# Kernel tuning notes

Hardware: AMD Instinct MI355X
Metric: run time of the kernel (lower is better)

The kernel has to match this reference:

```python
import jax, jax.numpy as jnp
import numpy as np


def color_bin(x, n_bins):
    """Per-image 3D color histogram over n_bins**3 flat bins.
    x: [B, 3, H, W] float in ~[-1, 1]. Returns [B, n_bins**3] float32.
    """
    B, C, H, W = x.shape
    n_tot = n_bins ** 3
    # torch color_bins: i*(2/n_bins) - 1 for i in 1..n_bins-1
    boundaries = jnp.arange(1, n_bins, dtype=jnp.float32) * (2.0 / n_bins) - 1.0
    # torch.bucketize(right=False) == searchsorted side='left'
    idx = jnp.searchsorted(boundaries, x.reshape(B, C, H * W), side='left')  # [B,3,HW] int
    scale = jnp.array([1, n_bins, n_bins ** 2], dtype=idx.dtype)
    flat = jnp.einsum('bcp,c->bp', idx, scale)  # [B, HW], values in [0, n_tot)
    # torch.histc(bins, n_tot, min=0, max=n_tot-1) on exact integers == bincount
    hist = jax.vmap(lambda f: jnp.bincount(f, length=n_tot))(flat)
    return hist.astype(jnp.float32) / (H * W)


def setup_inputs() -> dict:
    key = jax.random.key(0)
    k1, k2 = jax.random.split(key)
    inp = jax.random.normal(k1, (8, 3, 1024, 1024), dtype=jnp.float32)
    style = jax.random.normal(k2, (1, 3, 1024, 1024), dtype=jnp.float32)
    return {"input": inp, "style_image": style, "n_bins": 16}


def reference(input, style_image, n_bins):
    # target histogram from the style image (detached in torch; ints anyway)
    target = color_bin(style_image, n_bins).squeeze(0)  # [n_tot]
    cols = color_bin(input, n_bins)                     # [B, n_tot]
    # F.l1_loss(cols, target.repeat(B, 1)) with mean reduction
    loss = jnp.mean(jnp.abs(cols - target[None, :]))
    return loss
```

## Files before the change

kernel.cpp:

```cpp
#include <hip/hip_runtime.h>

#define HW      (1024 * 1024)
#define HW4     (HW / 4)
#define NBINS   4096
#define NIMG    9
#define BPI     256
#define THREADS 256
#define F4_PER_BLOCK (HW4 / BPI)
#define NPART   (NIMG * BPI)

typedef float f4 __attribute__((ext_vector_type(4)));

__device__ __forceinline__ int bin16(float x) {
    int lo = 0;
    if (0.0f < x) lo = 8;
    if ((float)(lo + 4) * 0.125f - 1.0f < x) lo += 4;
    if ((float)(lo + 2) * 0.125f - 1.0f < x) lo += 2;
    if ((float)(lo + 1) * 0.125f - 1.0f < x) lo += 1;
    return lo;
}

__device__ __forceinline__ int bin3(float r, float g, float b) {
    return bin16(r) + 16 * bin16(g) + 256 * bin16(b);
}

__device__ __forceinline__ void acc4(int* lh, f4 r, f4 g, f4 b) {
    atomicAdd(&lh[bin3(r.x, g.x, b.x)], 1);
    atomicAdd(&lh[bin3(r.y, g.y, b.y)], 1);
    atomicAdd(&lh[bin3(r.z, g.z, b.z)], 1);
    atomicAdd(&lh[bin3(r.w, g.w, b.w)], 1);
}

__global__ __launch_bounds__(THREADS) void hist_kernel(
        const float* __restrict__ input,
        const float* __restrict__ style,
        unsigned int* __restrict__ part) {
    __shared__ int lh[NBINS];
    const int img = blockIdx.y;
    const int blk = blockIdx.x;
    const float* base = (img < 8) ? (input + (size_t)img * 3 * HW) : style;

    for (int i = threadIdx.x; i < NBINS; i += THREADS) lh[i] = 0;
    __syncthreads();

    const f4* c0 = (const f4*)(base);
    const f4* c1 = (const f4*)(base + HW);
    const f4* c2 = (const f4*)(base + 2 * HW);
    const int start = blk * F4_PER_BLOCK;

    for (int j = threadIdx.x; j < F4_PER_BLOCK; j += 2 * THREADS) {
        const int p0 = start + j;
        const int p1 = p0 + THREADS;
        f4 r0 = c0[p0], g0 = c1[p0], b0 = c2[p0];
        f4 r1 = c0[p1], g1 = c1[p1], b1 = c2[p1];
        acc4(lh, r0, g0, b0);
        acc4(lh, r1, g1, b1);
    }
    __syncthreads();

    uint2* dst = (uint2*)(part + ((size_t)img * BPI + blk) * (NBINS / 2));
    for (int i = threadIdx.x; i < NBINS / 4; i += THREADS) {
        uint2 v;
        v.x = (unsigned)lh[4 * i]     | ((unsigned)lh[4 * i + 1] << 16);
        v.y = (unsigned)lh[4 * i + 2] | ((unsigned)lh[4 * i + 3] << 16);
        dst[i] = v;
    }
}

__global__ __launch_bounds__(THREADS) void reduce_kernel(
        const unsigned short* __restrict__ part,
        int* __restrict__ H2) {
    const int img  = blockIdx.y;
    const int half = blockIdx.z;
    const int bin  = blockIdx.x * THREADS + threadIdx.x;
    const unsigned short* p = part
        + ((size_t)img * BPI + half * (BPI / 2)) * NBINS + bin;
    int sum = 0;
#pragma unroll 16
    for (int b = 0; b < BPI / 2; ++b) sum += p[(size_t)b * NBINS];
    H2[((size_t)half * NIMG + img) * NBINS + bin] = sum;
}

__global__ __launch_bounds__(1024) void loss_kernel(
        const int* __restrict__ H2, float* __restrict__ out) {
    __shared__ int tgt_l[NBINS];
    __shared__ int partsum[16];
    const int* h0 = H2;
    const int* h1 = H2 + NIMG * NBINS;
    for (int i = threadIdx.x; i < NBINS; i += 1024)
        tgt_l[i] = h0[8 * NBINS + i] + h1[8 * NBINS + i];
    __syncthreads();

    int acc = 0;
    for (int e = threadIdx.x; e < 8 * NBINS; e += 1024) {
        const int c = h0[e] + h1[e];
        const int d = c - tgt_l[e & (NBINS - 1)];
        acc += (d < 0) ? -d : d;
    }
    for (int off = 32; off; off >>= 1) acc += __shfl_down(acc, off, 64);
    const int lane = threadIdx.x & 63;
    const int wv   = threadIdx.x >> 6;
    if (lane == 0) partsum[wv] = acc;
    __syncthreads();
    if (wv == 0) {
        int t = (lane < 16) ? partsum[lane] : 0;
        for (int off = 8; off; off >>= 1) t += __shfl_down(t, off, 64);
        if (lane == 0) {
            out[0] = (float)((double)(long long)t / 34359738368.0);
        }
    }
}

extern "C" void kernel_launch(void* const* d_in, const int* in_sizes, int n_in,
                              void* d_out, int out_size, void* d_ws, size_t ws_size,
                              hipStream_t stream) {
    const float* input = (const float*)d_in[0];
    const float* style = (const float*)d_in[1];
    unsigned int* part = (unsigned int*)d_ws;
    int* H2 = (int*)((char*)d_ws + (size_t)NPART * NBINS * sizeof(unsigned short));

    hipLaunchKernelGGL(hist_kernel, dim3(BPI, NIMG), dim3(THREADS), 0, stream,
                       input, style, part);
    hipLaunchKernelGGL(reduce_kernel, dim3(NBINS / THREADS, NIMG, 2),
                       dim3(THREADS), 0, stream,
                       (const unsigned short*)part, H2);
    hipLaunchKernelGGL(loss_kernel, dim3(1), dim3(1024), 0, stream,
                       H2, (float*)d_out);
}
```

Baseline: 179.9 us.

## Halve hist blocks per image and fuse partial reduction with L1 loss

```diff
diff --git a/kernel.cpp b/kernel.cpp
--- a/kernel.cpp
+++ b/kernel.cpp
@@ -4,10 +4,10 @@
 #define HW4     (HW / 4)
 #define NBINS   4096
 #define NIMG    9
-#define BPI     256
+#define BPI     128
 #define THREADS 256
 #define F4_PER_BLOCK (HW4 / BPI)
-#define NPART   (NIMG * BPI)
+#define RBINS   32
 
 typedef float f4 __attribute__((ext_vector_type(4)));
 
@@ -34,7 +34,7 @@
 __global__ __launch_bounds__(THREADS) void hist_kernel(
         const float* __restrict__ input,
         const float* __restrict__ style,
-        unsigned int* __restrict__ part) {
+        unsigned short* __restrict__ part) {
     __shared__ int lh[NBINS];
     const int img = blockIdx.y;
     const int blk = blockIdx.x;
@@ -58,57 +58,61 @@
     }
     __syncthreads();
 
-    uint2* dst = (uint2*)(part + ((size_t)img * BPI + blk) * (NBINS / 2));
-    for (int i = threadIdx.x; i < NBINS / 4; i += THREADS) {
-        uint2 v;
-        v.x = (unsigned)lh[4 * i]     | ((unsigned)lh[4 * i + 1] << 16);
-        v.y = (unsigned)lh[4 * i + 2] | ((unsigned)lh[4 * i + 3] << 16);
+    uint4* dst = (uint4*)(part + ((size_t)img * BPI + blk) * NBINS);
+    for (int i = threadIdx.x; i < NBINS / 8; i += THREADS) {
+        uint4 v;
+        v.x = (unsigned)lh[8 * i]     | ((unsigned)lh[8 * i + 1] << 16);
+        v.y = (unsigned)lh[8 * i + 2] | ((unsigned)lh[8 * i + 3] << 16);
+        v.z = (unsigned)lh[8 * i + 4] | ((unsigned)lh[8 * i + 5] << 16);
+        v.w = (unsigned)lh[8 * i + 6] | ((unsigned)lh[8 * i + 7] << 16);
         dst[i] = v;
     }
 }
 
-__global__ __launch_bounds__(THREADS) void reduce_kernel(
+__global__ __launch_bounds__(THREADS) void reduce_loss_kernel(
         const unsigned short* __restrict__ part,
-        int* __restrict__ H2) {
-    const int img  = blockIdx.y;
-    const int half = blockIdx.z;
-    const int bin  = blockIdx.x * THREADS + threadIdx.x;
-    const unsigned short* p = part
-        + ((size_t)img * BPI + half * (BPI / 2)) * NBINS + bin;
-    int sum = 0;
+        int* __restrict__ slots) {
+    __shared__ int red[8][RBINS];
+    __shared__ int tgt[RBINS];
+    const int b0   = blockIdx.x * RBINS;
+    const int lane = threadIdx.x & 31;
+    const int pg   = threadIdx.x >> 5;
+    int acc = 0;
+
+    for (int step = 0; step < NIMG; ++step) {
+        const int img = (step == 0) ? 8 : step - 1;
+        const unsigned short* p =
+            part + ((size_t)img * BPI + pg) * NBINS + b0 + lane;
+        int s = 0;
 #pragma unroll 16
-    for (int b = 0; b < BPI / 2; ++b) sum += p[(size_t)b * NBINS];
-    H2[((size_t)half * NIMG + img) * NBINS + bin] = sum;
+        for (int k = 0; k < BPI / 8; ++k)
+            s += p[(size_t)(8 * k) * NBINS];
+        red[pg][lane] = s;
+        __syncthreads();
+        if (threadIdx.x < RBINS) {
+            int tot = 0;
+#pragma unroll
+            for (int r = 0; r < 8; ++r) tot += red[r][threadIdx.x];
+            if (step == 0) {
+                tgt[threadIdx.x] = tot;
+            } else {
+                const int d = tot - tgt[threadIdx.x];
+                acc += (d < 0) ? -d : d;
+            }
+        }
+        __syncthreads();
+    }
+
+    for (int off = 32; off; off >>= 1) acc += __shfl_down(acc, off, 64);
+    if (threadIdx.x == 0) slots[blockIdx.x] = acc;
 }
 
-__global__ __launch_bounds__(1024) void loss_kernel(
-        const int* __restrict__ H2, float* __restrict__ out) {
-    __shared__ int tgt_l[NBINS];
-    __shared__ int partsum[16];
-    const int* h0 = H2;
-    const int* h1 = H2 + NIMG * NBINS;
-    for (int i = threadIdx.x; i < NBINS; i += 1024)
-        tgt_l[i] = h0[8 * NBINS + i] + h1[8 * NBINS + i];
-    __syncthreads();
-
-    int acc = 0;
-    for (int e = threadIdx.x; e < 8 * NBINS; e += 1024) {
-        const int c = h0[e] + h1[e];
-        const int d = c - tgt_l[e & (NBINS - 1)];
-        acc += (d < 0) ? -d : d;
-    }
-    for (int off = 32; off; off >>= 1) acc += __shfl_down(acc, off, 64);
-    const int lane = threadIdx.x & 63;
-    const int wv   = threadIdx.x >> 6;
-    if (lane == 0) partsum[wv] = acc;
-    __syncthreads();
-    if (wv == 0) {
-        int t = (lane < 16) ? partsum[lane] : 0;
-        for (int off = 8; off; off >>= 1) t += __shfl_down(t, off, 64);
-        if (lane == 0) {
-            out[0] = (float)((double)(long long)t / 34359738368.0);
-        }
-    }
+__global__ __launch_bounds__(64) void final_kernel(
+        const int* __restrict__ slots, float* __restrict__ out) {
+    const int t = threadIdx.x;
+    int s = slots[t] + slots[t + 64];
+    for (int off = 32; off; off >>= 1) s += __shfl_down(s, off, 64);
+    if (t == 0) out[0] = (float)((double)s / 34359738368.0);
 }
 
 extern "C" void kernel_launch(void* const* d_in, const int* in_sizes, int n_in,
@@ -116,14 +120,14 @@
                               hipStream_t stream) {
     const float* input = (const float*)d_in[0];
     const float* style = (const float*)d_in[1];
-    unsigned int* part = (unsigned int*)d_ws;
-    int* H2 = (int*)((char*)d_ws + (size_t)NPART * NBINS * sizeof(unsigned short));
+    unsigned short* part = (unsigned short*)d_ws;
+    int* slots = (int*)((char*)d_ws +
+                        (size_t)NIMG * BPI * NBINS * sizeof(unsigned short));
 
     hipLaunchKernelGGL(hist_kernel, dim3(BPI, NIMG), dim3(THREADS), 0, stream,
                        input, style, part);
-    hipLaunchKernelGGL(reduce_kernel, dim3(NBINS / THREADS, NIMG, 2),
-                       dim3(THREADS), 0, stream,
-                       (const unsigned short*)part, H2);
-    hipLaunchKernelGGL(loss_kernel, dim3(1), dim3(1024), 0, stream,
-                       H2, (float*)d_out);
+    hipLaunchKernelGGL(reduce_loss_kernel, dim3(NBINS / RBINS), dim3(THREADS),
+                       0, stream, part, slots);
+    hipLaunchKernelGGL(final_kernel, dim3(1), dim3(64), 0, stream,
+                       slots, (float*)d_out);
 }
```

Result: faster. 173.0 us (-3.8%).
